# Optimization experiments

Hardware: AMD Instinct MI355X
Metric: run time of the kernel (lower is better)

The kernel has to match this reference:

```python
import jax, jax.numpy as jnp
import numpy as np

B, T, IN_DIM, UNITS, PEAK_DIM = 64, 1024, 256, 512, 512


def setup_inputs() -> dict:
    key = jax.random.key(0)
    ks = jax.random.split(key, 6)
    s = lambda fan: 1.0 / np.sqrt(fan)
    return {
        "x": jax.random.normal(ks[0], (B, T, IN_DIM), dtype=jnp.float32),
        "peak": jax.random.normal(ks[1], (B, PEAK_DIM), dtype=jnp.float32),
        "kernel": jax.random.normal(ks[2], (IN_DIM, 3 * UNITS), dtype=jnp.float32) * s(IN_DIM),
        "recurrent_kernel": jax.random.normal(ks[3], (UNITS, 3 * UNITS), dtype=jnp.float32) * s(UNITS),
        "peak_kernel": jax.random.normal(ks[4], (PEAK_DIM, 3 * UNITS), dtype=jnp.float32) * s(PEAK_DIM),
        "bias": jnp.zeros((3 * UNITS,), dtype=jnp.float32),
        "peak_initial": jax.random.normal(ks[5], (PEAK_DIM, UNITS), dtype=jnp.float32) * s(PEAK_DIM),
    }


def _hard_sigmoid(a):
    # Keras hard_sigmoid: clip(0.2*x + 0.5, 0, 1)
    return jnp.clip(0.2 * a + 0.5, 0.0, 1.0)


def reference(x, peak, kernel, recurrent_kernel, peak_kernel, bias, peak_initial):
    U = peak_initial.shape[1]
    # Initial state from peak context: h0 = peak @ peak_initial  [B, U]
    h0 = jnp.dot(peak, peak_initial)
    # Precompute time-invariant projections (same math as per-step dots).
    xp = jnp.einsum("bti,ik->btk", x, kernel) + bias          # [B, T, 3U]
    pp = jnp.dot(peak, peak_kernel)                              # [B, 3U]

    def step(h, xt):
        hp = jnp.dot(h, recurrent_kernel)                        # [B, 3U]
        zr = _hard_sigmoid(xt[:, : 2 * U] + hp[:, : 2 * U] + pp[:, : 2 * U])
        z, r = zr[:, :U], zr[:, U:]
        hh = jnp.tanh(xt[:, 2 * U :] + r * (hp[:, 2 * U :] + pp[:, 2 * U :]))
        h_new = z * h + (1.0 - z) * hh
        return h_new, h_new

    xs = jnp.swapaxes(xp, 0, 1)                                  # [T, B, 3U]
    _, hs = jax.lax.scan(step, h0, xs)                           # [T, B, U]
    return jnp.swapaxes(hs, 0, 1)                                # [B, T, U]
```

## Files before the change

kernel.cpp:

```cpp
#include <hip/hip_runtime.h>
#include <hip/hip_bf16.h>

#define B_   64
#define T_   1024
#define IND_ 256
#define U_   512
#define G3_  1536
#define BPG   8
#define SLOTS 32

typedef unsigned int u32;
typedef unsigned short u16;
typedef unsigned long long u64;
typedef __attribute__((ext_vector_type(8))) short short8;
typedef __attribute__((ext_vector_type(4))) float f32x4;
typedef __attribute__((ext_vector_type(4))) unsigned int u32x4;

union S8 { short8 v; u16 us[8]; u32 d[4]; u64 q[2]; };
union BF { __hip_bfloat16 b; u16 u; };
union FU { float f; u32 u; };

__device__ __forceinline__ u16 f2b(float f){ BF t; t.b = __float2bfloat16(f); return t.u; }
__device__ __forceinline__ float b2f(u16 u){ FU t; t.u = ((u32)u) << 16; return t.f; }
__device__ __forceinline__ float hsig(float a){ return fminf(fmaxf(fmaf(a, 0.2f, 0.5f), 0.f), 1.f); }
__device__ __forceinline__ u32 umax2(u32 a, u32 b){ return a > b ? a : b; }
__device__ __forceinline__ float fast_tanh(float x){
  float ax = fabsf(x);
  float e  = __expf(ax + ax);
  float r  = 1.f - 2.f / (e + 1.f);
  return copysignf(r, x);
}
__device__ __forceinline__ void drain_vm(){
  asm volatile("s_waitcnt vmcnt(0)" ::: "memory");
  __builtin_amdgcn_sched_barrier(0);
}
__device__ __forceinline__ void st_sys(u32* p, u32 v){
  asm volatile("global_store_dword %0, %1, off sc0 sc1" :: "v"(p), "v"(v) : "memory");
}
__device__ __forceinline__ u32 ld_sys(const u32* p){
  u32 v;
  asm volatile("global_load_dword %0, %1, off sc0 sc1\n\ts_waitcnt vmcnt(0)"
               : "=v"(v) : "v"(p) : "memory");
  return v;
}

#define LDA16(aa, hb) \
  asm volatile( \
    "global_load_dwordx4 %0,  %16, off sc0 sc1\n\t" \
    "global_load_dwordx4 %1,  %16, off offset:64 sc0 sc1\n\t" \
    "global_load_dwordx4 %2,  %16, off offset:128 sc0 sc1\n\t" \
    "global_load_dwordx4 %3,  %16, off offset:192 sc0 sc1\n\t" \
    "global_load_dwordx4 %4,  %16, off offset:256 sc0 sc1\n\t" \
    "global_load_dwordx4 %5,  %16, off offset:320 sc0 sc1\n\t" \
    "global_load_dwordx4 %6,  %16, off offset:384 sc0 sc1\n\t" \
    "global_load_dwordx4 %7,  %16, off offset:448 sc0 sc1\n\t" \
    "global_load_dwordx4 %8,  %16, off offset:512 sc0 sc1\n\t" \
    "global_load_dwordx4 %9,  %16, off offset:576 sc0 sc1\n\t" \
    "global_load_dwordx4 %10, %16, off offset:640 sc0 sc1\n\t" \
    "global_load_dwordx4 %11, %16, off offset:704 sc0 sc1\n\t" \
    "global_load_dwordx4 %12, %16, off offset:768 sc0 sc1\n\t" \
    "global_load_dwordx4 %13, %16, off offset:832 sc0 sc1\n\t" \
    "global_load_dwordx4 %14, %16, off offset:896 sc0 sc1\n\t" \
    "global_load_dwordx4 %15, %16, off offset:960 sc0 sc1\n\t" \
    "s_waitcnt vmcnt(0)" \
    : "=&v"(aa[0].v),  "=&v"(aa[1].v),  "=&v"(aa[2].v),  "=&v"(aa[3].v), \
      "=&v"(aa[4].v),  "=&v"(aa[5].v),  "=&v"(aa[6].v),  "=&v"(aa[7].v), \
      "=&v"(aa[8].v),  "=&v"(aa[9].v),  "=&v"(aa[10].v), "=&v"(aa[11].v), \
      "=&v"(aa[12].v), "=&v"(aa[13].v), "=&v"(aa[14].v), "=&v"(aa[15].v) \
    : "v"(hb) : "memory")


__global__ void k_zero(u32* c) {
  int i = threadIdx.x;
  for (int k = i; k < 1024; k += 256) c[k] = 0u;
}

__global__ void k_fill(u32x4* p) {
  size_t i = (size_t)blockIdx.x * 256 + threadIdx.x;
  u32x4 v = {0xFFFFFFFFu, 0xFFFFFFFFu, 0xFFFFFFFFu, 0xFFFFFFFFu};
  p[i] = v;
}

__global__ void k_wt(const float* __restrict__ rk, const float* __restrict__ xk,
                     u16* __restrict__ WrT, u16* __restrict__ WxT) {
  int i = blockIdx.x * 256 + threadIdx.x;
  if (i < U_ * G3_) {
    int k = i / G3_, c = i - k * G3_;
    WrT[(size_t)c * U_ + k] = f2b(rk[i]);
  } else {
    int j = i - U_ * G3_;
    int k = j / G3_, c = j - k * G3_;
    WxT[(size_t)c * IND_ + k] = f2b(xk[j]);
  }
}

__global__ void k_xb(const float* __restrict__ x, u16* __restrict__ xb) {
  size_t i = ((size_t)blockIdx.x * 256 + threadIdx.x) * 8;
  const float4* p = (const float4*)(x + i);
  float4 a = p[0], b = p[1];
  S8 o;
  o.us[0]=f2b(a.x); o.us[1]=f2b(a.y); o.us[2]=f2b(a.z); o.us[3]=f2b(a.w);
  o.us[4]=f2b(b.x); o.us[5]=f2b(b.y); o.us[6]=f2b(b.z); o.us[7]=f2b(b.w);
  *(short8*)(xb + i) = o.v;
}

__global__ void k_pp(const float* __restrict__ peak, const float* __restrict__ pk,
                     float* __restrict__ pp) {
  int i = blockIdx.x * 256 + threadIdx.x;
  int b = i / G3_, c = i - b * G3_;
  const float* pr = peak + b * U_;
  float s = 0.f;
  for (int k = 0; k < U_; ++k) s = fmaf(pr[k], pk[(size_t)k * G3_ + c], s);
  pp[i] = s;
}

__global__ void k_h0b(const float* __restrict__ peak, const float* __restrict__ pi,
                      u16* __restrict__ hb0) {
  int i = blockIdx.x * 256 + threadIdx.x;
  int b = i >> 9, u = i & 511;
  const float* pr = peak + b * U_;
  float s = 0.f;
  for (int k = 0; k < U_; ++k) s = fmaf(pr[k], pi[(size_t)k * U_ + u], s);
  hb0[i] = f2b(s);
}

__global__ void k_h0(const float* __restrict__ peak, const float* __restrict__ pi,
                     float* __restrict__ h0, u16* __restrict__ hb0) {
  int i = blockIdx.x * 256 + threadIdx.x;
  int b = i >> 9, u = i & 511;
  const float* pr = peak + b * U_;
  float s = 0.f;
  for (int k = 0; k < U_; ++k) s = fmaf(pr[k], pi[(size_t)k * U_ + u], s);
  h0[i] = s;
  hb0[i] = f2b(s);
}


template<bool XBQ>
__global__ __launch_bounds__(64, 1) void k_scan_s(
    const void* __restrict__ xsrc, const float* __restrict__ bias,
    const float* __restrict__ pp,
    const u16* __restrict__ WrT, const u16* __restrict__ WxT,
    u16* __restrict__ hbuf, float* __restrict__ out)
{
  __shared__ short8 lB[4608];

  const int tid = threadIdx.x;
  const int g = blockIdx.x & 3;
  const int s = blockIdx.x >> 2;
  const int scol0 = s * 16;

  for (int lin = tid; lin < 3072; lin += 64) {
    int lp = lin & 63, ks = (lin >> 6) & 15, gate = lin >> 10;
    int cc = lp & 15, kk = lp >> 4;
    lB[lin] = *(const short8*)(WrT + (size_t)(gate * U_ + scol0 + cc) * U_ + ks * 32 + kk * 8);
  }
  for (int lin = tid; lin < 1536; lin += 64) {
    int lp = lin & 63, ks = (lin >> 6) & 7, gate = lin >> 9;
    int cc = lp & 15, kk = lp >> 4;
    lB[3072 + lin] = *(const short8*)(WxT + (size_t)(gate * U_ + scol0 + cc) * IND_ + ks * 32 + kk * 8);
  }
  __syncthreads();

  const int c   = tid & 15;
  const int kg  = tid >> 4;
  const int col = scol0 + c;

  float bpz[4], bpr[4], pph[4], hprev[4];
  float bh = bias[2 * U_ + col];
#pragma unroll
  for (int q = 0; q < 4; ++q) {
    int bg = g * 16 + kg * 4 + q;
    bpz[q]   = bias[col]       + pp[(size_t)bg * G3_ + col];
    bpr[q]   = bias[U_ + col]  + pp[(size_t)bg * G3_ + U_ + col];
    pph[q]   = pp[(size_t)bg * G3_ + 2 * U_ + col];
    hprev[q] = b2f(hbuf[(size_t)bg * U_ + col]);
  }

  const u16*   xbrow = (const u16*)xsrc   + (size_t)(g * 16 + c) * T_ * IND_;
  const float* xfrow = (const float*)xsrc + (size_t)(g * 16 + c) * T_ * IND_;
  const f32x4 z4 = {0.f, 0.f, 0.f, 0.f};
  f32x4 pxz, pxr, pxh;
  S8 xaA[8], xaB[8];

#define XLOAD(tt, XA) do { \
    if constexpr (XBQ) { \
      _Pragma("unroll") \
      for (int ks = 0; ks < 8; ++ks) \
        XA[ks].v = *(const short8*)(xbrow + (size_t)(tt) * IND_ + kg * 8 + ks * 32); \
    } else { \
      _Pragma("unroll") \
      for (int ks = 0; ks < 8; ++ks) { \
        const float4* p4_ = (const float4*)(xfrow + (size_t)(tt) * IND_ + kg * 8 + ks * 32); \
        float4 x0_ = p4_[0], x1_ = p4_[1]; \
        XA[ks].us[0]=f2b(x0_.x); XA[ks].us[1]=f2b(x0_.y); XA[ks].us[2]=f2b(x0_.z); XA[ks].us[3]=f2b(x0_.w); \
        XA[ks].us[4]=f2b(x1_.x); XA[ks].us[5]=f2b(x1_.y); XA[ks].us[6]=f2b(x1_.z); XA[ks].us[7]=f2b(x1_.w); \
      } \
    } \
  } while (0)

#define XMFMA(XA) do { \
    _Pragma("unroll") \
    for (int ks = 0; ks < 8; ++ks) { \
      pxz = __builtin_amdgcn_mfma_f32_16x16x32_bf16(XA[ks].v, lB[3072 + (0*8+ks)*64 + tid], pxz, 0,0,0); \
      pxr = __builtin_amdgcn_mfma_f32_16x16x32_bf16(XA[ks].v, lB[3072 + (1*8+ks)*64 + tid], pxr, 0,0,0); \
      pxh = __builtin_amdgcn_mfma_f32_16x16x32_bf16(XA[ks].v, lB[3072 + (2*8+ks)*64 + tid], pxh, 0,0,0); \
    } \
  } while (0)

  XLOAD(0, xaB);
  pxz = z4; pxr = z4; pxh = z4;
  XMFMA(xaB);
  XLOAD(1, xaA);

#define ONESTEP(t, XCN, XLD) do { \
    const u16* hb = hbuf + (size_t)(t) * (B_ * U_) + (size_t)(g * 16 + c) * U_ + kg * 8; \
    S8 aa[16]; \
    for (;;) { \
      LDA16(aa, hb); \
      u32 mx = 0; \
      _Pragma("unroll") \
      for (int ks = 0; ks < 16; ++ks) \
        mx = umax2(mx, umax2(umax2(aa[ks].d[0], aa[ks].d[1]), \
                             umax2(aa[ks].d[2], aa[ks].d[3]))); \
      if (__all((int)(mx < 0xFFFF0000u))) break; \
    } \
    if ((t) + 2 < T_) XLOAD((t) + 2, XLD);           \
    f32x4 az = pxz, ar = pxr, ah = pxh, ahr = z4; \
    _Pragma("unroll") \
    for (int ks = 0; ks < 16; ++ks) { \
      az  = __builtin_amdgcn_mfma_f32_16x16x32_bf16(aa[ks].v, lB[(0*16+ks)*64 + tid], az,  0,0,0); \
      ar  = __builtin_amdgcn_mfma_f32_16x16x32_bf16(aa[ks].v, lB[(1*16+ks)*64 + tid], ar,  0,0,0); \
      ahr = __builtin_amdgcn_mfma_f32_16x16x32_bf16(aa[ks].v, lB[(2*16+ks)*64 + tid], ahr, 0,0,0); \
    } \
    float hnew[4]; \
    _Pragma("unroll") \
    for (int q = 0; q < 4; ++q) { \
      float z  = hsig(az[q] + bpz[q]); \
      float r  = hsig(ar[q] + bpr[q]); \
      float hh = fast_tanh(ah[q] + bh + r * (ahr[q] + pph[q])); \
      hnew[q] = fmaf(z, hprev[q] - hh, hh); \
      hprev[q] = hnew[q]; \
    } \
    u16* hb1 = hbuf + (size_t)((t) + 1) * (B_ * U_); \
    _Pragma("unroll") \
    for (int q = 0; q < 4; ++q) { \
      u32 hv = (u32)f2b(hnew[q]); \
      u32 w0 = hv | ((u32)__shfl_xor((int)hv, 1) << 16); \
      u32 w1 = (u32)__shfl_xor((int)w0, 2); \
      u32 w2 = (u32)__shfl_xor((int)w0, 4); \
      u32 w3 = (u32)__shfl_xor((int)w1, 4); \
      if (!(c & 7)) { \
        u32x4 vv = {w0, w1, w2, w3}; \
        asm volatile("global_store_dwordx4 %0, %1, off sc0 sc1" \
                     :: "v"((u32*)(hb1 + (size_t)(g * 16 + kg * 4 + q) * U_ + scol0 + c)), "v"(vv) : "memory"); \
      } \
    } \
    _Pragma("unroll") \
    for (int q = 0; q < 4; ++q) { \
      int bg = g * 16 + kg * 4 + q; \
      out[((size_t)bg * T_ + (t)) * U_ + col] = hnew[q]; \
    } \
    if ((t) < T_ - 1) { pxz = z4; pxr = z4; pxh = z4; XMFMA(XCN); } \
  } while (0)

  for (int t = 0; t < T_; t += 2) {
    ONESTEP(t,     xaA, xaB);
    ONESTEP(t + 1, xaB, xaA);
  }
#undef ONESTEP
#undef XMFMA
#undef XLOAD
}


template<bool XBQ>
__global__ __launch_bounds__(64, 1) void k_scan_fb(
    const void* __restrict__ xsrc, const float* __restrict__ bias,
    const float* __restrict__ pp, const float* __restrict__ h0,
    const u16* __restrict__ WrT, const u16* __restrict__ WxT,
    u16* __restrict__ hbuf, u32* __restrict__ cnt, float* __restrict__ out)
{
  __shared__ short8 lB[4608];

  const int tid = threadIdx.x;
  const int g = blockIdx.x & 7;
  const int s = blockIdx.x >> 3;
  const int scol0 = s * 16;

  for (int lin = tid; lin < 3072; lin += 64) {
    int lp = lin & 63, ks = (lin >> 6) & 15, gate = lin >> 10;
    int cc = lp & 15, kk = lp >> 4;
    lB[lin] = *(const short8*)(WrT + (size_t)(gate * U_ + scol0 + cc) * U_ + ks * 32 + kk * 8);
  }
  for (int lin = tid; lin < 1536; lin += 64) {
    int lp = lin & 63, ks = (lin >> 6) & 7, gate = lin >> 9;
    int cc = lp & 15, kk = lp >> 4;
    lB[3072 + lin] = *(const short8*)(WxT + (size_t)(gate * U_ + scol0 + cc) * IND_ + ks * 32 + kk * 8);
  }
  __syncthreads();

  const int c = tid & 15, kg = tid >> 4;
  const int col = scol0 + c;
  const int kge = kg & 1;

  float bpz[4], bpr[4], pph[4], hprev[4];
  float bh = bias[2 * U_ + col];
#pragma unroll
  for (int q = 0; q < 4; ++q) {
    int bg = g * BPG + kge * 4 + q;
    bpz[q]   = bias[col]       + pp[(size_t)bg * G3_ + col];
    bpr[q]   = bias[U_ + col]  + pp[(size_t)bg * G3_ + U_ + col];
    pph[q]   = pp[(size_t)bg * G3_ + 2 * U_ + col];
    hprev[q] = h0[(size_t)bg * U_ + col];
  }

  u16* hbA = hbuf + (size_t)(g * 2 + 0) * BPG * U_;
  u16* hbB = hbuf + (size_t)(g * 2 + 1) * BPG * U_;
  u32* cntp  = cnt + g * 32;
  u32* flags = cnt + 256 + g * 64;
  const u32* fp = flags + (tid & 31);

#pragma unroll
  for (int q = 0; q < 4; ++q) {
    u32 hv = (u32)f2b(hprev[q]);
    u32 ov = (u32)__shfl_xor((int)hv, 1);
    if (kg < 2 && !(c & 1))
      __hip_atomic_store((u32*)(hbA + (size_t)(kg * 4 + q) * U_ + col), hv | (ov << 16),
                         __ATOMIC_RELAXED, __HIP_MEMORY_SCOPE_AGENT);
  }
  drain_vm();
  if (tid == 0)
    __hip_atomic_fetch_add(cntp, 1u, __ATOMIC_RELAXED, __HIP_MEMORY_SCOPE_AGENT);

  const u16*   xbrow = (const u16*)xsrc   + (size_t)(g * BPG + (c & 7)) * T_ * IND_;
  const float* xfrow = (const float*)xsrc + (size_t)(g * BPG + (c & 7)) * T_ * IND_;
  const f32x4 z4 = {0.f, 0.f, 0.f, 0.f};
  f32x4 pxz = z4, pxr = z4, pxh = z4;

#define GEMM_XFB(tt, AZ, AR, AH) do { \
    _Pragma("unroll") \
    for (int ks = 0; ks < 8; ++ks) { \
      S8 a_; \
      if constexpr (XBQ) { \
        a_.v = *(const short8*)(xbrow + (size_t)(tt) * IND_ + kg * 8 + ks * 32); \
      } else { \
        const float4* p4_ = (const float4*)(xfrow + (size_t)(tt) * IND_ + kg * 8 + ks * 32); \
        float4 x0_ = p4_[0], x1_ = p4_[1]; \
        a_.us[0]=f2b(x0_.x); a_.us[1]=f2b(x0_.y); a_.us[2]=f2b(x0_.z); a_.us[3]=f2b(x0_.w); \
        a_.us[4]=f2b(x1_.x); a_.us[5]=f2b(x1_.y); a_.us[6]=f2b(x1_.z); a_.us[7]=f2b(x1_.w); \
      } \
      AZ = __builtin_amdgcn_mfma_f32_16x16x32_bf16(a_.v, lB[3072 + (0*8+ks)*64 + tid], AZ, 0,0,0); \
      AR = __builtin_amdgcn_mfma_f32_16x16x32_bf16(a_.v, lB[3072 + (1*8+ks)*64 + tid], AR, 0,0,0); \
      AH = __builtin_amdgcn_mfma_f32_16x16x32_bf16(a_.v, lB[3072 + (2*8+ks)*64 + tid], AH, 0,0,0); \
    } \
  } while (0)

  GEMM_XFB(0, pxz, pxr, pxh);

  while (__hip_atomic_load(cntp, __ATOMIC_RELAXED, __HIP_MEMORY_SCOPE_AGENT) < (u32)SLOTS)
    __builtin_amdgcn_s_sleep(1);

  for (int t = 0; t < T_; ++t) {
    const u16* hb = ((t & 1) ? hbB : hbA) + (size_t)(c & 7) * U_ + kg * 8;
    S8 aa[16];
    LDA16(aa, hb);

    f32x4 az = pxz, ar = pxr, ah = pxh, ahr = z4;
#pragma unroll
    for (int ks = 0; ks < 16; ++ks) {
      az  = __builtin_amdgcn_mfma_f32_16x16x32_bf16(aa[ks].v, lB[(0*16+ks)*64 + tid], az,  0,0,0);
      ar  = __builtin_amdgcn_mfma_f32_16x16x32_bf16(aa[ks].v, lB[(1*16+ks)*64 + tid], ar,  0,0,0);
      ahr = __builtin_amdgcn_mfma_f32_16x16x32_bf16(aa[ks].v, lB[(2*16+ks)*64 + tid], ahr, 0,0,0);
    }

    float hnew[4];
#pragma unroll
    for (int q = 0; q < 4; ++q) {
      float z = hsig(az[q] + bpz[q]);
      float r = hsig(ar[q] + bpr[q]);
      float hh = fast_tanh(ah[q] + bh + r * (ahr[q] + pph[q]));
      hnew[q] = fmaf(z, hprev[q] - hh, hh);
      hprev[q] = hnew[q];
    }

    u16* ho = (t & 1) ? hbA : hbB;
#pragma unroll
    for (int q = 0; q < 4; ++q) {
      u32 hv = (u32)f2b(hnew[q]);
      u32 ov = (u32)__shfl_xor((int)hv, 1);
      if (kg < 2 && !(c & 1))
        __hip_atomic_store((u32*)(ho + (size_t)(kg * 4 + q) * U_ + col), hv | (ov << 16),
                           __ATOMIC_RELAXED, __HIP_MEMORY_SCOPE_AGENT);
    }
    drain_vm();
    if (tid == 0) st_sys((u32*)(flags + s), (u32)(t + 1));

    if (t < T_ - 1) {
      pxz = z4; pxr = z4; pxh = z4;
      GEMM_XFB(t + 1, pxz, pxr, pxh);
    }
    if (kg < 2) {
#pragma unroll
      for (int q = 0; q < 4; ++q) {
        int bg = g * BPG + kg * 4 + q;
        out[((size_t)bg * T_ + t) * U_ + col] = hnew[q];
      }
    }
    if (t < T_ - 1) {
      u32 target = (u32)(t + 1);
      while (true) {
        u32 v = ld_sys(fp);
        if (__all((int)(v >= target))) break;
        __builtin_amdgcn_s_sleep(1);
      }
    }
  }
#undef GEMM_XFB
}


extern "C" void kernel_launch(void* const* d_in, const int* in_sizes, int n_in,
                              void* d_out, int out_size, void* d_ws, size_t ws_size,
                              hipStream_t stream) {
  const float* x    = (const float*)d_in[0];
  const float* peak = (const float*)d_in[1];
  const float* xk   = (const float*)d_in[2];
  const float* rk   = (const float*)d_in[3];
  const float* pk   = (const float*)d_in[4];
  const float* bias = (const float*)d_in[5];
  const float* pi   = (const float*)d_in[6];
  float* out = (float*)d_out;

  char* w = (char*)d_ws;
  u16*   WrT = (u16*)(w);
  u16*   WxT = (u16*)(w + 1572864);
  float* pp  = (float*)(w + 2359296);

  const size_t HBUF_BYTES = (size_t)(T_ + 1) * B_ * U_ * 2;
  const size_t NEED_S_F32 = (size_t)2752512 + HBUF_BYTES;
  const size_t NEED_S_XB  = NEED_S_F32 + 33554432;
  const size_t NEED_FB_XB = (size_t)36573184;

  k_wt<<<dim3(4608), dim3(256), 0, stream>>>(rk, xk, WrT, WxT);
  k_pp<<<dim3(384),  dim3(256), 0, stream>>>(peak, pk, pp);

  if (ws_size >= NEED_S_F32) {
    u16* hbuf = (u16*)(w + 2752512);
    k_fill<<<dim3(16400), dim3(256), 0, stream>>>((u32x4*)hbuf);
    k_h0b <<<dim3(128),   dim3(256), 0, stream>>>(peak, pi, hbuf);
    if (ws_size >= NEED_S_XB) {
      u16* xb = (u16*)(w + 69926912);
      k_xb<<<dim3(8192), dim3(256), 0, stream>>>(x, xb);
      k_scan_s<true><<<dim3(128), dim3(64), 0, stream>>>(xb, bias, pp, WrT, WxT, hbuf, out);
    } else {
      k_scan_s<false><<<dim3(128), dim3(64), 0, stream>>>(x, bias, pp, WrT, WxT, hbuf, out);
    }
  } else {
    float* h0   = (float*)(w + 2752512);
    u16*   hbuf = (u16*)(w + 2883584);
    u32*   cnt  = (u32*)(w + 3014656);
    k_zero<<<dim3(1),   dim3(256), 0, stream>>>(cnt);
    k_h0  <<<dim3(128), dim3(256), 0, stream>>>(peak, pi, h0, hbuf);
    if (ws_size >= NEED_FB_XB) {
      u16* xb = (u16*)(w + 3018752);
      k_xb<<<dim3(8192), dim3(256), 0, stream>>>(x, xb);
      k_scan_fb<true><<<dim3(256), dim3(64), 0, stream>>>(xb, bias, pp, h0, WrT, WxT, hbuf, cnt, out);
    } else {
      k_scan_fb<false><<<dim3(256), dim3(64), 0, stream>>>(x, bias, pp, h0, WrT, WxT, hbuf, cnt, out);
    }
  }
}
```

Measured before the change: 3.065 ms.

## Move fp32 output writes out of scan into separate bf16-to-fp32 expansion kernel

The recurrent scan kernel no longer writes fp32 outputs each timestep; it only stores the bf16 hidden state into the history buffer, now as packed dword stores after a single shuffle. A new bandwidth-bound kernel afterwards expands the whole bf16 history into the fp32 output tensor. This takes large strided global writes off the serial per-step critical path. The cost is an extra pass over the output and outputs rounded to bf16 precision.

```diff
diff --git a/kernel.cpp b/kernel.cpp
--- a/kernel.cpp
+++ b/kernel.cpp
@@ -135,13 +135,29 @@
   hb0[i] = f2b(s);
 }
 
+__global__ void k_out(const u16* __restrict__ hbuf, float* __restrict__ out) {
+  size_t i = ((size_t)blockIdx.x * 256 + threadIdx.x) * 8;
+  size_t b = i >> 19;
+  size_t r = i & 524287;
+  size_t t = r >> 9;
+  size_t u = r & 511;
+  S8 v;
+  v.v = *(const short8*)(hbuf + (t + 1) * (size_t)(B_ * U_) + b * U_ + u);
+  float4 o0, o1;
+  o0.x = b2f(v.us[0]); o0.y = b2f(v.us[1]); o0.z = b2f(v.us[2]); o0.w = b2f(v.us[3]);
+  o1.x = b2f(v.us[4]); o1.y = b2f(v.us[5]); o1.z = b2f(v.us[6]); o1.w = b2f(v.us[7]);
+  float4* dst = (float4*)(out + i);
+  dst[0] = o0;
+  dst[1] = o1;
+}
+
 
 template<bool XBQ>
 __global__ __launch_bounds__(64, 1) void k_scan_s(
     const void* __restrict__ xsrc, const float* __restrict__ bias,
     const float* __restrict__ pp,
     const u16* __restrict__ WrT, const u16* __restrict__ WxT,
-    u16* __restrict__ hbuf, float* __restrict__ out)
+    u16* __restrict__ hbuf)
 {
   __shared__ short8 lB[4608];
 
@@ -246,20 +262,9 @@
     _Pragma("unroll") \
     for (int q = 0; q < 4; ++q) { \
       u32 hv = (u32)f2b(hnew[q]); \
-      u32 w0 = hv | ((u32)__shfl_xor((int)hv, 1) << 16); \
-      u32 w1 = (u32)__shfl_xor((int)w0, 2); \
-      u32 w2 = (u32)__shfl_xor((int)w0, 4); \
-      u32 w3 = (u32)__shfl_xor((int)w1, 4); \
-      if (!(c & 7)) { \
-        u32x4 vv = {w0, w1, w2, w3}; \
-        asm volatile("global_store_dwordx4 %0, %1, off sc0 sc1" \
-                     :: "v"((u32*)(hb1 + (size_t)(g * 16 + kg * 4 + q) * U_ + scol0 + c)), "v"(vv) : "memory"); \
-      } \
-    } \
-    _Pragma("unroll") \
-    for (int q = 0; q < 4; ++q) { \
-      int bg = g * 16 + kg * 4 + q; \
-      out[((size_t)bg * T_ + (t)) * U_ + col] = hnew[q]; \
+      u32 ov = (u32)__shfl_xor((int)hv, 1); \
+      if (!(c & 1)) \
+        st_sys((u32*)(hb1 + (size_t)(g * 16 + kg * 4 + q) * U_ + col), hv | (ov << 16)); \
     } \
     if ((t) < T_ - 1) { pxz = z4; pxr = z4; pxh = z4; XMFMA(XCN); } \
   } while (0)
@@ -452,10 +457,11 @@
     if (ws_size >= NEED_S_XB) {
       u16* xb = (u16*)(w + 69926912);
       k_xb<<<dim3(8192), dim3(256), 0, stream>>>(x, xb);
-      k_scan_s<true><<<dim3(128), dim3(64), 0, stream>>>(xb, bias, pp, WrT, WxT, hbuf, out);
+      k_scan_s<true><<<dim3(128), dim3(64), 0, stream>>>(xb, bias, pp, WrT, WxT, hbuf);
     } else {
-      k_scan_s<false><<<dim3(128), dim3(64), 0, stream>>>(x, bias, pp, WrT, WxT, hbuf, out);
-    }
+      k_scan_s<false><<<dim3(128), dim3(64), 0, stream>>>(x, bias, pp, WrT, WxT, hbuf);
+    }
+    k_out<<<dim3(16384), dim3(256), 0, stream>>>(hbuf, out);
   } else {
     float* h0   = (float*)(w + 2752512);
     u16*   hbuf = (u16*)(w + 2883584);
```

Result: faster. 2.902 ms (median of 2 runs) (-5.3%).
